# Kernel tuning notes

Measured on AMD Instinct MI355X. Metric: run time of the kernel, lower is better.

Reference implementation:

```python
import jax, jax.numpy as jnp
import numpy as np

N, FEAT, EMB, OUT = 16384, 256, 128, 128


def setup_inputs() -> dict:
    key = jax.random.key(0)
    k1, k2, k3, k4, k5 = jax.random.split(key, 5)
    s1 = 1.0 / np.sqrt(FEAT)
    s2 = 1.0 / np.sqrt(EMB)
    return {
        "x": jax.random.normal(k1, (N, FEAT), dtype=jnp.float32),
        "W1": jax.random.uniform(k2, (FEAT, EMB), jnp.float32, -s1, s1),
        "b1": jax.random.uniform(k3, (EMB,), jnp.float32, -s1, s1),
        "W2": jax.random.uniform(k4, (EMB, OUT), jnp.float32, -s2, s2),
        "b2": jax.random.uniform(k5, (OUT,), jnp.float32, -s2, s2),
    }


def reference(x, W1, b1, W2, b2):
    # projection: [N, feat] -> [N, emb]
    h = x @ W1 + b1
    # dense self-similarity graph: A_ = h h^T  (N x N)
    A_ = h @ h.T
    # degree-style normalization: A_ij -> 2*A_ij / (A_ii + A_jj)
    d = jnp.diagonal(A_)  # [N], == row squared norms of h
    A = 2.0 * A_ / (d[:, None] + d[None, :])
    # degree-normalized aggregation then output MLP + ReLU
    agg = A @ h  # [N, emb]
    return jax.nn.relu(agg @ W2 + b2)
```

## Files before the change

### kernel.cpp

```cpp
#include <hip/hip_runtime.h>
#include <stdint.h>

#define N_TOK 16384
#define FEAT  256
#define EMB   128
#define NQ    11
#define KC    16

typedef float  f32x4  __attribute__((ext_vector_type(4)));
typedef __bf16 bf16x8 __attribute__((ext_vector_type(8)));
typedef short  s16x8  __attribute__((ext_vector_type(8)));
typedef unsigned int u32x4 __attribute__((ext_vector_type(4)));

__device__ __forceinline__ unsigned short bf16_rne(float f) {
    union { float f; unsigned u; } v; v.f = f;
    unsigned u = v.u;
    return (unsigned short)((u + 0x7FFFu + ((u >> 16) & 1u)) >> 16);
}
__device__ __forceinline__ float bf16_to_f32(unsigned short s) {
    union { unsigned u; float f; } v; v.u = ((unsigned)s) << 16; return v.f;
}
__device__ __forceinline__ unsigned pack_trunc(float a, float b) {
    union { float f; unsigned u; } ua, ub; ua.f = a; ub.f = b;
    return (ub.u & 0xFFFF0000u) | (ua.u >> 16);
}
__device__ __forceinline__ unsigned pack_rne(float a, float b) {
    return (unsigned)bf16_rne(a) | ((unsigned)bf16_rne(b) << 16);
}
__device__ __forceinline__ void async_cp16(const void* g, void* l) {
    __builtin_amdgcn_global_load_lds(
        (const __attribute__((address_space(1))) unsigned int*)g,
        (__attribute__((address_space(3))) unsigned int*)l, 16, 0, 0);
}

__global__ void k0_transpose(const float* __restrict__ W1, const float* __restrict__ W2,
                             unsigned short* __restrict__ W1T, unsigned short* __restrict__ W2T)
{
    const int tid  = blockIdx.x * blockDim.x + threadIdx.x;
    const int nthr = gridDim.x * blockDim.x;
    for (int i = tid; i < FEAT * EMB; i += nthr) {
        const int r = i >> 7, c = i & 127;
        W1T[c * FEAT + r] = bf16_rne(W1[i]);
    }
    for (int i = tid; i < EMB * EMB; i += nthr) {
        const int r = i >> 7, c = i & 127;
        W2T[c * EMB + r] = bf16_rne(W2[i]);
    }
}

__global__ __launch_bounds__(256) void k1_proj(
    const float* __restrict__ x, const unsigned short* __restrict__ W1T,
    const float* __restrict__ b1,
    unsigned short* __restrict__ h, unsigned short* __restrict__ hT,
    float* __restrict__ UT)
{
    __shared__ __align__(16) unsigned char W1s[65536];
    __shared__ unsigned short ldsT[128 * 68];
    const int lane = threadIdx.x & 63;
    const int wave = threadIdx.x >> 6;
    const int quad = lane >> 4;
    const int l15  = lane & 15;
    const int arow = blockIdx.x * 64 + wave * 16 + l15;

    float4 xv[16];
    #pragma unroll
    for (int ks = 0; ks < 8; ++ks) {
        const float* xp = x + (size_t)arow * FEAT + ks * 32 + quad * 8;
        xv[2 * ks]     = *(const float4*)xp;
        xv[2 * ks + 1] = *(const float4*)(xp + 4);
    }
    #pragma unroll
    for (int c = 0; c < 16; ++c) {
        const int chunk = wave * 16 + c;
        const int row = chunk * 2 + (lane >> 5);
        const int b = (lane & 31) ^ (row & 15);
        async_cp16(W1T + (size_t)row * FEAT + b * 8, W1s + chunk * 1024);
    }
    bf16x8 afr[8];
    #pragma unroll
    for (int ks = 0; ks < 8; ++ks) {
        const float4 xa = xv[2 * ks], xb = xv[2 * ks + 1];
        s16x8 at;
        at[0] = (short)bf16_rne(xa.x); at[1] = (short)bf16_rne(xa.y);
        at[2] = (short)bf16_rne(xa.z); at[3] = (short)bf16_rne(xa.w);
        at[4] = (short)bf16_rne(xb.x); at[5] = (short)bf16_rne(xb.y);
        at[6] = (short)bf16_rne(xb.z); at[7] = (short)bf16_rne(xb.w);
        afr[ks] = __builtin_bit_cast(bf16x8, at);
    }
    __syncthreads();

    const f32x4 zero4 = {0.f, 0.f, 0.f, 0.f};
    f32x4 acc[8];
    #pragma unroll
    for (int n0 = 0; n0 < 8; ++n0) acc[n0] = zero4;
    #pragma unroll
    for (int ks = 0; ks < 8; ++ks)
        #pragma unroll
        for (int n0 = 0; n0 < 8; ++n0) {
            const int n = n0 * 16 + l15;
            const int b = (ks * 4 + quad) ^ (n & 15);
            const bf16x8 bfr = *(const bf16x8*)(W1s + n * 512 + b * 16);
            acc[n0] = __builtin_amdgcn_mfma_f32_16x16x32_bf16(afr[ks], bfr, acc[n0], 0, 0, 0);
        }

    const int rbase = blockIdx.x * 64 + wave * 16 + quad * 4;
    float dpart[4] = {0.f, 0.f, 0.f, 0.f};
    #pragma unroll
    for (int n0 = 0; n0 < 8; ++n0) {
        const int col = n0 * 16 + l15;
        const float bias = b1[col];
        unsigned short hb[4];
        #pragma unroll
        for (int r = 0; r < 4; ++r) {
            const float hv = acc[n0][r] + bias;
            const unsigned short q = bf16_rne(hv);
            hb[r] = q;
            const float bb = bf16_to_f32(q);
            dpart[r] += bb * bb;
            h[(size_t)(rbase + r) * EMB + col] = q;
        }
        ushort4 pk = make_ushort4(hb[0], hb[1], hb[2], hb[3]);
        *(ushort4*)&ldsT[col * 68 + wave * 16 + quad * 4] = pk;
    }
    const float tql = __expf(0.9f * (float)l15 - 10.8f);
    #pragma unroll
    for (int r = 0; r < 4; ++r) {
        float v = dpart[r];
        v += __shfl_xor(v, 1);
        v += __shfl_xor(v, 2);
        v += __shfl_xor(v, 4);
        v += __shfl_xor(v, 8);
        if (l15 < 10)       UT[(size_t)l15 * N_TOK + rbase + r] = __expf(-tql * v);
        else if (l15 == 10) UT[(size_t)10  * N_TOK + rbase + r] = 1.0f;
    }
    __syncthreads();
    const int rbase0 = blockIdx.x * 64;
    #pragma unroll
    for (int i = 0; i < 4; ++i) {
        const int slot = i * 256 + threadIdx.x;
        const int c    = slot >> 3;
        const int seg  = slot & 7;
        const ushort4 a0 = *(const ushort4*)&ldsT[c * 68 + seg * 8];
        const ushort4 a1 = *(const ushort4*)&ldsT[c * 68 + seg * 8 + 4];
        ushort4 o[2] = {a0, a1};
        *(uint4*)&hT[(size_t)c * N_TOK + rbase0 + seg * 8] = *(const uint4*)o;
    }
}

#define K2A_STAGE(sub_, dst_) do {                                              \
    const int kwin_ = kc * 1024 + (sub_) * 128;                                 \
    _Pragma("unroll")                                                           \
    for (int c = 0; c < 8; ++c) {                                               \
        const int chunk = wave * 8 + c;                                         \
        const int row = chunk * 4 + (lane >> 4);                                \
        const int b = (lane & 15) ^ (row & 15);                                 \
        async_cp16(hT + (size_t)row * N_TOK + kwin_ + b * 8, (dst_) + chunk * 1024); \
    } } while (0)

__global__ __launch_bounds__(256, 2) void k2a_gram(
    const unsigned short* __restrict__ hT, const float* __restrict__ UT,
    float* __restrict__ Gp)
{
    __shared__ __align__(16) unsigned char Rb[2][32768];
    const int lane = threadIdx.x & 63;
    const int wave = threadIdx.x >> 6;
    const int quad = lane >> 4;
    const int l15  = lane & 15;
    const int q  = blockIdx.x >> 5;
    const int kc = (blockIdx.x >> 1) & 15;
    const int F  = blockIdx.x & 1;
    const int E  = wave;

    const f32x4 zero4 = {0.f, 0.f, 0.f, 0.f};
    f32x4 acc[2][4];
    #pragma unroll
    for (int mt = 0; mt < 2; ++mt)
        #pragma unroll
        for (int nt = 0; nt < 4; ++nt) acc[mt][nt] = zero4;

    K2A_STAGE(0, Rb[0]);
    __syncthreads();

    #pragma unroll 1
    for (int sub = 0; sub < 8; ++sub) {
        if (sub < 7) K2A_STAGE(sub + 1, Rb[(sub + 1) & 1]);
        const unsigned char* rb = Rb[sub & 1];
        const int kwin = kc * 1024 + sub * 128;

        #pragma unroll
        for (int ks = 0; ks < 4; ++ks) {
            const int kb = kwin + ks * 32 + quad * 8;
            const float4 ua = *(const float4*)(UT + (size_t)q * N_TOK + kb);
            const float4 ub = *(const float4*)(UT + (size_t)q * N_TOK + kb + 4);
            const float uv[8] = {ua.x, ua.y, ua.z, ua.w, ub.x, ub.y, ub.z, ub.w};
            bf16x8 au[2];
            #pragma unroll
            for (int mt = 0; mt < 2; ++mt) {
                const int re = E * 32 + mt * 16 + l15;
                const int b = (ks * 4 + quad) ^ (re & 15);
                const s16x8 raw = *(const s16x8*)(rb + re * 256 + b * 16);
                u32x4 ww;
                #pragma unroll
                for (int w = 0; w < 4; ++w) {
                    const float fa = bf16_to_f32((unsigned short)raw[2 * w])     * uv[2 * w];
                    const float fb = bf16_to_f32((unsigned short)raw[2 * w + 1]) * uv[2 * w + 1];
                    ww[w] = pack_trunc(fa, fb);
                }
                au[mt] = __builtin_bit_cast(bf16x8, ww);
            }
            #pragma unroll
            for (int nt = 0; nt < 4; ++nt) {
                const int rf = F * 64 + nt * 16 + l15;
                const int b = (ks * 4 + quad) ^ (rf & 15);
                const bf16x8 bfr = *(const bf16x8*)(rb + rf * 256 + b * 16);
                #pragma unroll
                for (int mt = 0; mt < 2; ++mt)
                    acc[mt][nt] = __builtin_amdgcn_mfma_f32_16x16x32_bf16(au[mt], bfr, acc[mt][nt], 0, 0, 0);
            }
        }
        if (sub < 7) __syncthreads();
    }

    float* gp = Gp + (size_t)(q * KC + kc) * (EMB * EMB);
    #pragma unroll
    for (int mt = 0; mt < 2; ++mt)
        #pragma unroll
        for (int nt = 0; nt < 4; ++nt)
            #pragma unroll
            for (int r = 0; r < 4; ++r)
                gp[(size_t)(E * 32 + mt * 16 + quad * 4 + r) * EMB + F * 64 + nt * 16 + l15] = acc[mt][nt][r];
}

__global__ __launch_bounds__(256) void k2b_gwt(
    const float* __restrict__ Gp, const unsigned short* __restrict__ W2T,
    unsigned short* __restrict__ GWT)
{
    __shared__ __align__(16) unsigned char Gs[16 * 256];
    const int q  = blockIdx.x >> 3;
    const int fs = blockIdx.x & 7;
    const int tid = threadIdx.x;

    {
        const int fg  = tid >> 4;
        const int blk = tid & 15;
        const float* src = Gp + (size_t)q * KC * (EMB * EMB)
                              + (size_t)(fs * 16 + fg) * EMB + blk * 8;
        float s[8] = {0.f, 0.f, 0.f, 0.f, 0.f, 0.f, 0.f, 0.f};
        #pragma unroll
        for (int kc = 0; kc < KC; ++kc) {
            const float4 a = *(const float4*)(src + (size_t)kc * (EMB * EMB));
            const float4 b = *(const float4*)(src + (size_t)kc * (EMB * EMB) + 4);
            s[0] += a.x; s[1] += a.y; s[2] += a.z; s[3] += a.w;
            s[4] += b.x; s[5] += b.y; s[6] += b.z; s[7] += b.w;
        }
        u32x4 w;
        w[0] = pack_rne(s[0], s[1]);
        w[1] = pack_rne(s[2], s[3]);
        w[2] = pack_rne(s[4], s[5]);
        w[3] = pack_rne(s[6], s[7]);
        *(u32x4*)(Gs + fg * 256 + ((blk ^ fg) << 4)) = w;
    }
    __syncthreads();

    const int lane = tid & 63;
    const int wave = tid >> 6;
    const int quad = lane >> 4;
    const int l15  = lane & 15;
    const float scale = (q == 10) ? 2.0f * __expf(-10.8f)
                                  : 1.8f * __expf(0.9f * (float)q - 10.8f);

    const f32x4 zero4 = {0.f, 0.f, 0.f, 0.f};
    f32x4 acc[2];
    acc[0] = zero4; acc[1] = zero4;
    #pragma unroll
    for (int ks = 0; ks < 4; ++ks) {
        const int b = (ks * 4 + quad) ^ l15;
        const bf16x8 bfr = *(const bf16x8*)(Gs + l15 * 256 + b * 16);
        #pragma unroll
        for (int mt = 0; mt < 2; ++mt) {
            const int o = wave * 32 + mt * 16 + l15;
            const bf16x8 afr = *(const bf16x8*)(W2T + (size_t)o * EMB + ks * 32 + quad * 8);
            acc[mt] = __builtin_amdgcn_mfma_f32_16x16x32_bf16(afr, bfr, acc[mt], 0, 0, 0);
        }
    }
    #pragma unroll
    for (int mt = 0; mt < 2; ++mt)
        #pragma unroll
        for (int r = 0; r < 4; ++r)
            GWT[(size_t)q * (EMB * EMB) + (size_t)(wave * 32 + mt * 16 + quad * 4 + r) * EMB + fs * 16 + l15]
                = bf16_rne(acc[mt][r] * scale);
}

__global__ __launch_bounds__(256, 4) void k2c_apply(
    const unsigned short* __restrict__ h, const unsigned short* __restrict__ GWT,
    const float* __restrict__ UT, const float* __restrict__ b2,
    float* __restrict__ out)
{
    __shared__ __align__(16) unsigned char Gs[2][16384];
    const int lane = threadIdx.x & 63;
    const int wave = threadIdx.x >> 6;
    const int quad = lane >> 4;
    const int l15  = lane & 15;
    const int ih   = wave & 1;
    const int oh   = wave >> 1;
    const int i0   = (blockIdx.x >> 1) * 32;
    const int o0   = (blockIdx.x & 1) * 64;
    const int irow = i0 + ih * 16 + l15;

    bf16x8 araw[4];
    #pragma unroll
    for (int ks = 0; ks < 4; ++ks)
        araw[ks] = *(const bf16x8*)(h + (size_t)irow * EMB + ks * 32 + quad * 8);

    const f32x4 zero4 = {0.f, 0.f, 0.f, 0.f};
    f32x4 acc[2];
    acc[0] = zero4; acc[1] = zero4;

    #pragma unroll
    for (int c = 0; c < 4; ++c) {
        const int chunk = wave * 4 + c;
        const int row = chunk * 4 + quad;
        const int b = l15 ^ (row & 15);
        async_cp16(GWT + (size_t)(o0 + row) * EMB + b * 8, &Gs[0][chunk * 1024]);
    }
    #pragma unroll 1
    for (int q = 0; q < NQ; ++q) {
        __syncthreads();
        if (q + 1 < NQ) {
            const unsigned short* src = GWT + (size_t)(q + 1) * (EMB * EMB);
            unsigned char* dst = Gs[(q + 1) & 1];
            #pragma unroll
            for (int c = 0; c < 4; ++c) {
                const int chunk = wave * 4 + c;
                const int row = chunk * 4 + quad;
                const int b = l15 ^ (row & 15);
                async_cp16(src + (size_t)(o0 + row) * EMB + b * 8, dst + chunk * 1024);
            }
        }
        const float4 uq = *(const float4*)(UT + (size_t)q * N_TOK + i0 + ih * 16 + quad * 4);
        const unsigned char* gb = Gs[q & 1];
        #pragma unroll
        for (int nt = 0; nt < 2; ++nt) {
            const int ol = oh * 32 + nt * 16 + l15;
            f32x4 t = zero4;
            #pragma unroll
            for (int ks = 0; ks < 4; ++ks) {
                const int b = (ks * 4 + quad) ^ (ol & 15);
                const bf16x8 bfr = *(const bf16x8*)(gb + ol * 256 + b * 16);
                t = __builtin_amdgcn_mfma_f32_16x16x32_bf16(araw[ks], bfr, t, 0, 0, 0);
            }
            acc[nt][0] += uq.x * t[0];
            acc[nt][1] += uq.y * t[1];
            acc[nt][2] += uq.z * t[2];
            acc[nt][3] += uq.w * t[3];
        }
    }

    #pragma unroll
    for (int nt = 0; nt < 2; ++nt) {
        const int o = o0 + oh * 32 + nt * 16 + l15;
        const float bias = b2[o];
        #pragma unroll
        for (int r = 0; r < 4; ++r) {
            const float v = acc[nt][r] + bias;
            out[(size_t)(i0 + ih * 16 + quad * 4 + r) * EMB + o] = v > 0.f ? v : 0.f;
        }
    }
}

extern "C" void kernel_launch(void* const* d_in, const int* in_sizes, int n_in,
                              void* d_out, int out_size, void* d_ws, size_t ws_size,
                              hipStream_t stream) {
    const float* x  = (const float*)d_in[0];
    const float* W1 = (const float*)d_in[1];
    const float* b1 = (const float*)d_in[2];
    const float* W2 = (const float*)d_in[3];
    const float* b2 = (const float*)d_in[4];
    float* out = (float*)d_out;

    char* ws = (char*)d_ws;
    unsigned short* h   = (unsigned short*)(ws);
    unsigned short* hT  = (unsigned short*)(ws + 4194304);
    unsigned short* W1T = (unsigned short*)(ws + 8388608);
    unsigned short* W2T = (unsigned short*)(ws + 8454144);
    float*          UT  = (float*)        (ws + 8486912);
    float*          Gp  = (float*)        (ws + 9338880);
    unsigned short* GWT = (unsigned short*)(ws + 23920640);

    k0_transpose<<<dim3(64),          dim3(256), 0, stream>>>(W1, W2, W1T, W2T);
    k1_proj     <<<dim3(256),         dim3(256), 0, stream>>>(x, W1T, b1, h, hT, UT);
    k2a_gram    <<<dim3(NQ * KC * 2), dim3(256), 0, stream>>>(hT, UT, Gp);
    k2b_gwt     <<<dim3(NQ * 8),      dim3(256), 0, stream>>>(Gp, W2T, GWT);
    k2c_apply   <<<dim3(1024),        dim3(256), 0, stream>>>(h, GWT, UT, b2, out);
}
```

Before: 117.8 us.

## Exploit Gram matrix symmetry to compute only three of four 64x64 blocks

```diff
diff --git a/kernel.cpp b/kernel.cpp
--- a/kernel.cpp
+++ b/kernel.cpp
@@ -149,12 +149,12 @@
 
 #define K2A_STAGE(sub_, dst_) do {                                              \
     const int kwin_ = kc * 1024 + (sub_) * 128;                                 \
-    _Pragma("unroll")                                                           \
-    for (int c = 0; c < 8; ++c) {                                               \
-        const int chunk = wave * 8 + c;                                         \
-        const int row = chunk * 4 + (lane >> 4);                                \
-        const int b = (lane & 15) ^ (row & 15);                                 \
-        async_cp16(hT + (size_t)row * N_TOK + kwin_ + b * 8, (dst_) + chunk * 1024); \
+    for (int c = 0; c < nchw; ++c) {                                            \
+        const int chunk = wave * nchw + c;                                      \
+        const int lrow = chunk * 4 + (lane >> 4);                               \
+        const int b = (lane & 15) ^ (lrow & 15);                                \
+        async_cp16(hT + (size_t)(stagebase + lrow) * N_TOK + kwin_ + b * 8,     \
+                   (dst_) + chunk * 1024);                                      \
     } } while (0)
 
 __global__ __launch_bounds__(256, 2) void k2a_gram(
@@ -166,17 +166,19 @@
     const int wave = threadIdx.x >> 6;
     const int quad = lane >> 4;
     const int l15  = lane & 15;
-    const int q  = blockIdx.x >> 5;
-    const int kc = (blockIdx.x >> 1) & 15;
-    const int F  = blockIdx.x & 1;
-    const int E  = wave;
+    const int bid  = blockIdx.x;
+    const int q    = bid / (KC * 3);
+    const int rem  = bid - q * (KC * 3);
+    const int kc   = rem / 3;
+    const int t    = rem - kc * 3;
+    const int stagebase = (t == 2) ? 64 : 0;
+    const int nchw = (t == 1) ? 8 : 4;
+    const int boff = (t == 1) ? 64 : 0;
 
     const f32x4 zero4 = {0.f, 0.f, 0.f, 0.f};
-    f32x4 acc[2][4];
-    #pragma unroll
-    for (int mt = 0; mt < 2; ++mt)
-        #pragma unroll
-        for (int nt = 0; nt < 4; ++nt) acc[mt][nt] = zero4;
+    f32x4 acc[4];
+    #pragma unroll
+    for (int nt = 0; nt < 4; ++nt) acc[nt] = zero4;
 
     K2A_STAGE(0, Rb[0]);
     __syncthreads();
@@ -193,42 +195,34 @@
             const float4 ua = *(const float4*)(UT + (size_t)q * N_TOK + kb);
             const float4 ub = *(const float4*)(UT + (size_t)q * N_TOK + kb + 4);
             const float uv[8] = {ua.x, ua.y, ua.z, ua.w, ub.x, ub.y, ub.z, ub.w};
-            bf16x8 au[2];
-            #pragma unroll
-            for (int mt = 0; mt < 2; ++mt) {
-                const int re = E * 32 + mt * 16 + l15;
-                const int b = (ks * 4 + quad) ^ (re & 15);
-                const s16x8 raw = *(const s16x8*)(rb + re * 256 + b * 16);
-                u32x4 ww;
-                #pragma unroll
-                for (int w = 0; w < 4; ++w) {
-                    const float fa = bf16_to_f32((unsigned short)raw[2 * w])     * uv[2 * w];
-                    const float fb = bf16_to_f32((unsigned short)raw[2 * w + 1]) * uv[2 * w + 1];
-                    ww[w] = pack_trunc(fa, fb);
-                }
-                au[mt] = __builtin_bit_cast(bf16x8, ww);
-            }
+            const int re = wave * 16 + l15;
+            const int ba = (ks * 4 + quad) ^ (re & 15);
+            const s16x8 raw = *(const s16x8*)(rb + re * 256 + ba * 16);
+            u32x4 ww;
+            #pragma unroll
+            for (int w = 0; w < 4; ++w) {
+                const float fa = bf16_to_f32((unsigned short)raw[2 * w])     * uv[2 * w];
+                const float fb = bf16_to_f32((unsigned short)raw[2 * w + 1]) * uv[2 * w + 1];
+                ww[w] = pack_trunc(fa, fb);
+            }
+            const bf16x8 au = __builtin_bit_cast(bf16x8, ww);
             #pragma unroll
             for (int nt = 0; nt < 4; ++nt) {
-                const int rf = F * 64 + nt * 16 + l15;
-                const int b = (ks * 4 + quad) ^ (rf & 15);
-                const bf16x8 bfr = *(const bf16x8*)(rb + rf * 256 + b * 16);
-                #pragma unroll
-                for (int mt = 0; mt < 2; ++mt)
-                    acc[mt][nt] = __builtin_amdgcn_mfma_f32_16x16x32_bf16(au[mt], bfr, acc[mt][nt], 0, 0, 0);
+                const int rf = boff + nt * 16 + l15;
+                const int bb = (ks * 4 + quad) ^ (rf & 15);
+                const bf16x8 bfr = *(const bf16x8*)(rb + rf * 256 + bb * 16);
+                acc[nt] = __builtin_amdgcn_mfma_f32_16x16x32_bf16(au, bfr, acc[nt], 0, 0, 0);
             }
         }
         if (sub < 7) __syncthreads();
     }
 
-    float* gp = Gp + (size_t)(q * KC + kc) * (EMB * EMB);
-    #pragma unroll
-    for (int mt = 0; mt < 2; ++mt)
-        #pragma unroll
-        for (int nt = 0; nt < 4; ++nt)
-            #pragma unroll
-            for (int r = 0; r < 4; ++r)
-                gp[(size_t)(E * 32 + mt * 16 + quad * 4 + r) * EMB + F * 64 + nt * 16 + l15] = acc[mt][nt][r];
+    float* gp = Gp + (size_t)((q * KC + kc) * 3 + t) * 4096;
+    #pragma unroll
+    for (int nt = 0; nt < 4; ++nt)
+        #pragma unroll
+        for (int r = 0; r < 4; ++r)
+            gp[(wave * 16 + quad * 4 + r) * 64 + nt * 16 + l15] = acc[nt][r];
 }
 
 __global__ __launch_bounds__(256) void k2b_gwt(
@@ -243,15 +237,38 @@
     {
         const int fg  = tid >> 4;
         const int blk = tid & 15;
-        const float* src = Gp + (size_t)q * KC * (EMB * EMB)
-                              + (size_t)(fs * 16 + fg) * EMB + blk * 8;
+        const int fgG = fs * 16 + fg;
+        const float* base0 = Gp + (size_t)q * (KC * 3) * 4096;
         float s[8] = {0.f, 0.f, 0.f, 0.f, 0.f, 0.f, 0.f, 0.f};
-        #pragma unroll
-        for (int kc = 0; kc < KC; ++kc) {
-            const float4 a = *(const float4*)(src + (size_t)kc * (EMB * EMB));
-            const float4 b = *(const float4*)(src + (size_t)kc * (EMB * EMB) + 4);
-            s[0] += a.x; s[1] += a.y; s[2] += a.z; s[3] += a.w;
-            s[4] += b.x; s[5] += b.y; s[6] += b.z; s[7] += b.w;
+        if (fs < 4) {
+            const int t   = (blk < 8) ? 0 : 1;
+            const int off = fgG * 64 + (blk & 7) * 8;
+            #pragma unroll
+            for (int kc = 0; kc < KC; ++kc) {
+                const float* p = base0 + (size_t)(kc * 3 + t) * 4096 + off;
+                const float4 a = *(const float4*)p;
+                const float4 b = *(const float4*)(p + 4);
+                s[0] += a.x; s[1] += a.y; s[2] += a.z; s[3] += a.w;
+                s[4] += b.x; s[5] += b.y; s[6] += b.z; s[7] += b.w;
+            }
+        } else if (blk >= 8) {
+            const int off = (fgG - 64) * 64 + (blk - 8) * 8;
+            #pragma unroll
+            for (int kc = 0; kc < KC; ++kc) {
+                const float* p = base0 + (size_t)(kc * 3 + 2) * 4096 + off;
+                const float4 a = *(const float4*)p;
+                const float4 b = *(const float4*)(p + 4);
+                s[0] += a.x; s[1] += a.y; s[2] += a.z; s[3] += a.w;
+                s[4] += b.x; s[5] += b.y; s[6] += b.z; s[7] += b.w;
+            }
+        } else {
+            const int col = fgG - 64;
+            #pragma unroll
+            for (int kc = 0; kc < KC; ++kc) {
+                const float* p = base0 + (size_t)(kc * 3 + 1) * 4096 + blk * 8 * 64 + col;
+                #pragma unroll
+                for (int j = 0; j < 8; ++j) s[j] += p[j * 64];
+            }
         }
         u32x4 w;
         w[0] = pack_rne(s[0], s[1]);
@@ -389,7 +406,7 @@
 
     k0_transpose<<<dim3(64),          dim3(256), 0, stream>>>(W1, W2, W1T, W2T);
     k1_proj     <<<dim3(256),         dim3(256), 0, stream>>>(x, W1T, b1, h, hT, UT);
-    k2a_gram    <<<dim3(NQ * KC * 2), dim3(256), 0, stream>>>(hT, UT, Gp);
+    k2a_gram    <<<dim3(NQ * KC * 3), dim3(256), 0, stream>>>(hT, UT, Gp);
     k2b_gwt     <<<dim3(NQ * 8),      dim3(256), 0, stream>>>(Gp, W2T, GWT);
     k2c_apply   <<<dim3(1024),        dim3(256), 0, stream>>>(h, GWT, UT, b2, out);
 }
```

Result: slower. 129.6 us (+10.0%).
